# Kernel optimization log

Hardware: AMD Instinct MI355X
Metric: run time of the kernel (lower is better)

Reference implementation:

```python
import jax, jax.numpy as jnp
import numpy as np

H = 512      # hidden_size
E = 300      # embed_size
V = 50257    # output_size / vocab
B = 64       # batch
S = 128      # src_len
NEG = -1e10


def setup_inputs() -> dict:
    key = jax.random.key(0)
    ks = jax.random.split(key, 12)
    inp = {
        "input_ids": jax.random.randint(ks[0], (B,), 0, V),
        "hidden": jax.random.normal(ks[1], (B, H), jnp.float32),
        "encoder_outputs": jax.random.normal(ks[2], (S, B, 2 * H), jnp.float32),
        "mask": jax.random.randint(ks[3], (B, S), 0, 2).astype(jnp.int32),
        # parameters
        "emb_table": jax.random.normal(ks[4], (V, E), jnp.float32) * 0.02,
        "W_attn": jax.random.normal(ks[5], (H, 3 * H), jnp.float32) * 0.02,
        "b_attn": jnp.zeros((H,), jnp.float32),
        "v_w": jax.random.normal(ks[6], (1, H), jnp.float32) * 0.02,
        "W_ih": jax.random.normal(ks[7], (3 * H, 2 * H + E), jnp.float32) * 0.02,
        "W_hh": jax.random.normal(ks[8], (3 * H, H), jnp.float32) * 0.02,
        "b_ih": jnp.zeros((3 * H,), jnp.float32),
        "b_hh": jnp.zeros((3 * H,), jnp.float32),
        "W_out": jax.random.normal(ks[9], (V, 3 * H + E), jnp.float32) * 0.02,
        "b_out": jnp.zeros((V,), jnp.float32),
    }
    return inp


def reference(input_ids, hidden, encoder_outputs, mask,
              emb_table, W_attn, b_attn, v_w,
              W_ih, W_hh, b_ih, b_hh, W_out, b_out):
    # embedding lookup (dropout prob = 0 -> identity)
    embedded = emb_table[input_ids]                       # [B, E]

    # Bahdanau attention
    enc_b = jnp.transpose(encoder_outputs, (1, 0, 2))     # [B, S, 2H]
    hid_rep = jnp.broadcast_to(hidden[:, None, :], (hidden.shape[0], enc_b.shape[1], hidden.shape[1]))
    energy = jnp.tanh(jnp.concatenate([hid_rep, enc_b], axis=2) @ W_attn.T + b_attn)  # [B, S, H]
    scores = jnp.einsum('bsh,h->bs', energy, v_w[0])      # [B, S]
    scores = jnp.where(mask == 0, NEG, scores)
    a = jax.nn.softmax(scores, axis=1)                    # [B, S]

    # context vector
    weighted = jnp.einsum('bs,bse->be', a, enc_b)         # [B, 2H]

    # single-step GRU (PyTorch gate order: r, z, n)
    x = jnp.concatenate([embedded, weighted], axis=1)     # [B, E + 2H]
    gx = x @ W_ih.T + b_ih                                # [B, 3H]
    gh = hidden @ W_hh.T + b_hh                           # [B, 3H]
    h = hidden.shape[1]
    r = jax.nn.sigmoid(gx[:, :h] + gh[:, :h])
    z = jax.nn.sigmoid(gx[:, h:2*h] + gh[:, h:2*h])
    n = jnp.tanh(gx[:, 2*h:] + r * gh[:, 2*h:])
    h_new = (1.0 - z) * n + z * hidden                    # [B, H]

    # output projection
    prediction = jnp.concatenate([h_new, weighted, embedded], axis=1) @ W_out.T + b_out  # [B, V]
    return prediction, h_new, a
```

## Files before the change

### kernel.cpp

```cpp
#include <hip/hip_runtime.h>

typedef unsigned short ushort_t;
typedef short bf16x8 __attribute__((ext_vector_type(8)));
typedef float f32x4 __attribute__((ext_vector_type(4)));

#define B_ 64
#define H_ 512
#define E_ 300
#define V_ 50257
#define S_ 128

#define HNEW_OFS ((size_t)64 * 50257)
#define A_OFS    ((size_t)64 * 50257 + 64 * 512)

__device__ __forceinline__ unsigned short f2b(float f) {
  unsigned int u = __builtin_bit_cast(unsigned int, f);
  u = u + 0x7FFFu + ((u >> 16) & 1u);
  return (unsigned short)(u >> 16);
}
__device__ __forceinline__ float fast_tanh(float x) {
  x = fminf(15.f, fmaxf(-15.f, x));
  float e = __expf(-2.f * x);
  return (1.f - e) / (1.f + e);
}
__device__ __forceinline__ float fast_sigmoid(float x) {
  return 1.f / (1.f + __expf(-x));
}

template <int DT> struct Raw4;
template <> struct Raw4<0> {
  ushort4 v;
  __device__ static Raw4 zero() { return {make_ushort4(0, 0, 0, 0)}; }
};
template <> struct Raw4<1> {
  float4 v;
  __device__ static Raw4 zero() { return {make_float4(0.f, 0.f, 0.f, 0.f)}; }
};
template <int DT>
__device__ __forceinline__ Raw4<DT> ld_raw(const void* p, size_t off);
template <>
__device__ __forceinline__ Raw4<0> ld_raw<0>(const void* p, size_t off) {
  return {*(const ushort4*)((const ushort_t*)p + off)};
}
template <>
__device__ __forceinline__ Raw4<1> ld_raw<1>(const void* p, size_t off) {
  return {*(const float4*)((const float*)p + off)};
}
template <int DT>
__device__ __forceinline__ ushort4 to_b4(Raw4<DT> r);
template <>
__device__ __forceinline__ ushort4 to_b4<0>(Raw4<0> r) { return r.v; }
template <>
__device__ __forceinline__ ushort4 to_b4<1>(Raw4<1> r) {
  return make_ushort4(f2b(r.v.x), f2b(r.v.y), f2b(r.v.z), f2b(r.v.w));
}

template <int DTA, int DTW>
__global__ __launch_bounds__(256) void gemm_tile(
    const void* __restrict__ A, int lda,
    const void* __restrict__ W, int ldw, int wofs,
    const float* __restrict__ bias,
    float* __restrict__ C, int ldc,
    int M, int N, int K)
{
  __shared__ ushort_t sA[64 * 40];
  __shared__ ushort_t sB[64 * 40];
  const int tid = threadIdx.x;
  const int n0 = blockIdx.x * 64, m0 = blockIdx.y * 64;
  const int wave = tid >> 6, lane = tid & 63, quad = lane >> 4, l16 = lane & 15;

  f32x4 acc[4];
  #pragma unroll
  for (int i = 0; i < 4; ++i) acc[i] = (f32x4){0.f, 0.f, 0.f, 0.f};

  Raw4<DTA> ra[2];
  Raw4<DTW> rb[2];
  auto fetch = [&](int kt) {
    #pragma unroll
    for (int i = 0; i < 2; ++i) {
      int g = tid + i * 256;
      int row = g >> 3, gc = (g & 7) << 2;
      int gk = kt * 32 + gc;
      int ar = m0 + row, wr = n0 + row;
      ra[i] = Raw4<DTA>::zero();
      rb[i] = Raw4<DTW>::zero();
      if (gk < K && ar < M) ra[i] = ld_raw<DTA>(A, (size_t)ar * lda + gk);
      if (gk < K && wr < N) rb[i] = ld_raw<DTW>(W, (size_t)wr * ldw + wofs + gk);
    }
  };
  const int ksteps = (K + 31) >> 5;
  fetch(0);
  for (int kt = 0; kt < ksteps; ++kt) {
    #pragma unroll
    for (int i = 0; i < 2; ++i) {
      int g = tid + i * 256;
      int row = g >> 3, gc = (g & 7) << 2;
      *(ushort4*)(sA + row * 40 + gc) = to_b4<DTA>(ra[i]);
      *(ushort4*)(sB + row * 40 + gc) = to_b4<DTW>(rb[i]);
    }
    __syncthreads();
    if (kt + 1 < ksteps) fetch(kt + 1);
    bf16x8 af = *(const bf16x8*)(sA + (wave * 16 + l16) * 40 + quad * 8);
    #pragma unroll
    for (int nt = 0; nt < 4; ++nt) {
      bf16x8 bfr = *(const bf16x8*)(sB + (nt * 16 + l16) * 40 + quad * 8);
      acc[nt] = __builtin_amdgcn_mfma_f32_16x16x32_bf16(af, bfr, acc[nt], 0, 0, 0);
    }
    __syncthreads();
  }
  #pragma unroll
  for (int nt = 0; nt < 4; ++nt) {
    #pragma unroll
    for (int reg = 0; reg < 4; ++reg) {
      int row = m0 + wave * 16 + quad * 4 + reg;
      int col = n0 + nt * 16 + l16;
      if (row < M && col < N)
        C[(size_t)row * ldc + col] = acc[nt][reg] + bias[col];
    }
  }
}

__global__ __launch_bounds__(256) void attn_scores(
    const float* __restrict__ enc,
    const float* __restrict__ Wattn,
    const float* __restrict__ Gh,
    const float* __restrict__ vw,
    float* __restrict__ scores_part)
{
  __shared__ ushort_t sA[64 * 40];
  __shared__ ushort_t sB[64 * 40];
  const int tid = threadIdx.x;
  const int n0 = blockIdx.x * 64, m0 = blockIdx.y * 64;
  const int wave = tid >> 6, lane = tid & 63, quad = lane >> 4, l16 = lane & 15;

  f32x4 acc[4];
  #pragma unroll
  for (int i = 0; i < 4; ++i) acc[i] = (f32x4){0.f, 0.f, 0.f, 0.f};

  float4 ra[2], rb[2];
  auto fetch = [&](int kt) {
    #pragma unroll
    for (int i = 0; i < 2; ++i) {
      int g = tid + i * 256;
      int row = g >> 3, gc = (g & 7) << 2;
      int gk = kt * 32 + gc;
      ra[i] = *(const float4*)(enc + (size_t)(m0 + row) * 1024 + gk);
      rb[i] = *(const float4*)(Wattn + (size_t)(n0 + row) * 1536 + 512 + gk);
    }
  };
  fetch(0);
  for (int kt = 0; kt < 32; ++kt) {
    #pragma unroll
    for (int i = 0; i < 2; ++i) {
      int g = tid + i * 256;
      int row = g >> 3, gc = (g & 7) << 2;
      *(ushort4*)(sA + row * 40 + gc) =
          make_ushort4(f2b(ra[i].x), f2b(ra[i].y), f2b(ra[i].z), f2b(ra[i].w));
      *(ushort4*)(sB + row * 40 + gc) =
          make_ushort4(f2b(rb[i].x), f2b(rb[i].y), f2b(rb[i].z), f2b(rb[i].w));
    }
    __syncthreads();
    if (kt + 1 < 32) fetch(kt + 1);
    bf16x8 af = *(const bf16x8*)(sA + (wave * 16 + l16) * 40 + quad * 8);
    #pragma unroll
    for (int nt = 0; nt < 4; ++nt) {
      bf16x8 bfr = *(const bf16x8*)(sB + (nt * 16 + l16) * 40 + quad * 8);
      acc[nt] = __builtin_amdgcn_mfma_f32_16x16x32_bf16(af, bfr, acc[nt], 0, 0, 0);
    }
    __syncthreads();
  }
  float psum[4] = {0.f, 0.f, 0.f, 0.f};
  #pragma unroll
  for (int nt = 0; nt < 4; ++nt) {
    int h = n0 + nt * 16 + l16;
    float vh = vw[h];
    #pragma unroll
    for (int reg = 0; reg < 4; ++reg) {
      int r = m0 + wave * 16 + quad * 4 + reg;
      int b = r & 63;
      float e = acc[nt][reg] + Gh[b * 512 + h];
      psum[reg] += vh * fast_tanh(e);
    }
  }
  #pragma unroll
  for (int reg = 0; reg < 4; ++reg) {
    float p = psum[reg];
    p += __shfl_xor(p, 1);
    p += __shfl_xor(p, 2);
    p += __shfl_xor(p, 4);
    p += __shfl_xor(p, 8);
    if (l16 == 0) {
      int r = m0 + wave * 16 + quad * 4 + reg;
      scores_part[blockIdx.x * 8192 + r] = p;
    }
  }
}

__global__ __launch_bounds__(256) void softmax_ctx(
    const float* __restrict__ scores_part,
    const int* __restrict__ mask,
    const float* __restrict__ enc,
    const float* __restrict__ emb,
    const int* __restrict__ ids,
    float* __restrict__ out,
    ushort_t* __restrict__ x,
    ushort_t* __restrict__ xo)
{
  __shared__ float sc[128];
  __shared__ float red[128];
  const int b = blockIdx.x;
  const int tid = threadIdx.x;

  if (tid < 128) {
    float s = 0.f;
    #pragma unroll
    for (int nb = 0; nb < 8; ++nb) s += scores_part[nb * 8192 + tid * 64 + b];
    if (mask[b * 128 + tid] == 0) s = -1e10f;
    sc[tid] = s;
    red[tid] = s;
  }
  __syncthreads();
  for (int off = 64; off > 0; off >>= 1) {
    if (tid < off) red[tid] = fmaxf(red[tid], red[tid + off]);
    __syncthreads();
  }
  float m = red[0];
  __syncthreads();
  if (tid < 128) {
    float e = __expf(sc[tid] - m);
    sc[tid] = e;
    red[tid] = e;
  }
  __syncthreads();
  for (int off = 64; off > 0; off >>= 1) {
    if (tid < off) red[tid] += red[tid + off];
    __syncthreads();
  }
  float inv = 1.f / red[0];
  if (tid < 128) {
    float av = sc[tid] * inv;
    sc[tid] = av;
    out[A_OFS + b * 128 + tid] = av;
  }
  __syncthreads();

  {
    int e0 = tid * 4;
    float a0 = 0.f, a1 = 0.f, a2 = 0.f, a3 = 0.f;
    for (int s = 0; s < 128; ++s) {
      float as = sc[s];
      float4 ev = *(const float4*)(enc + (size_t)(s * 64 + b) * 1024 + e0);
      a0 += as * ev.x;
      a1 += as * ev.y;
      a2 += as * ev.z;
      a3 += as * ev.w;
    }
    ushort4 wb = make_ushort4(f2b(a0), f2b(a1), f2b(a2), f2b(a3));
    *(ushort4*)(x + b * 1344 + 300 + e0) = wb;
    *(ushort4*)(xo + b * 1856 + 512 + e0) = wb;
  }

  int rid = ids[b];
  for (int e = tid; e < 300; e += 256) {
    ushort_t h = f2b(emb[(size_t)rid * 300 + e]);
    x[b * 1344 + e] = h;
    xo[b * 1856 + 1536 + e] = h;
  }
  if (tid < 20) {
    x[b * 1344 + 1324 + tid] = 0;
    xo[b * 1856 + 1836 + tid] = 0;
  }
}

__global__ __launch_bounds__(256) void gru_pointwise(
    const float* __restrict__ gx,
    const float* __restrict__ gh,
    const float* __restrict__ hidden,
    float* __restrict__ out,
    ushort_t* __restrict__ xo)
{
  int i = blockIdx.x * 256 + threadIdx.x;
  int b = i >> 9, h = i & 511;
  float r = fast_sigmoid(gx[b * 1536 + h] + gh[b * 1536 + h]);
  float z = fast_sigmoid(gx[b * 1536 + 512 + h] + gh[b * 1536 + 512 + h]);
  float n = fast_tanh(gx[b * 1536 + 1024 + h] + r * gh[b * 1536 + 1024 + h]);
  float hp = hidden[b * 512 + h];
  float hn = (1.f - z) * n + z * hp;
  out[HNEW_OFS + b * 512 + h] = hn;
  xo[b * 1856 + h] = f2b(hn);
}

__global__ __launch_bounds__(256) void out_proj(
    const ushort_t* __restrict__ Xo,
    const float* __restrict__ Wout,
    const float* __restrict__ bout,
    float* __restrict__ pred)
{
  __shared__ ushort_t sA[64 * 40];
  __shared__ ushort_t sB[64 * 40];
  const int tid = threadIdx.x;
  const int n0 = blockIdx.x * 64;
  const int wave = tid >> 6, lane = tid & 63, quad = lane >> 4, l16 = lane & 15;

  f32x4 acc[4];
  #pragma unroll
  for (int i = 0; i < 4; ++i) acc[i] = (f32x4){0.f, 0.f, 0.f, 0.f};

  ushort4 ra[2];
  float4 rb[2];
  auto fetch = [&](int kt) {
    #pragma unroll
    for (int i = 0; i < 2; ++i) {
      int g = tid + i * 256;
      int row = g >> 3, gc = (g & 7) << 2;
      int gk = kt * 32 + gc;
      ra[i] = make_ushort4(0, 0, 0, 0);
      rb[i] = make_float4(0.f, 0.f, 0.f, 0.f);
      if (gk < 1836) {
        ra[i] = *(const ushort4*)(Xo + (size_t)row * 1856 + gk);
        int wr = n0 + row;
        if (wr < V_) rb[i] = *(const float4*)(Wout + (size_t)wr * 1836 + gk);
      }
    }
  };
  fetch(0);
  for (int kt = 0; kt < 58; ++kt) {
    #pragma unroll
    for (int i = 0; i < 2; ++i) {
      int g = tid + i * 256;
      int row = g >> 3, gc = (g & 7) << 2;
      *(ushort4*)(sA + row * 40 + gc) = ra[i];
      *(ushort4*)(sB + row * 40 + gc) =
          make_ushort4(f2b(rb[i].x), f2b(rb[i].y), f2b(rb[i].z), f2b(rb[i].w));
    }
    __syncthreads();
    if (kt + 1 < 58) fetch(kt + 1);
    bf16x8 af = *(const bf16x8*)(sA + (wave * 16 + l16) * 40 + quad * 8);
    #pragma unroll
    for (int nt = 0; nt < 4; ++nt) {
      bf16x8 bfr = *(const bf16x8*)(sB + (nt * 16 + l16) * 40 + quad * 8);
      acc[nt] = __builtin_amdgcn_mfma_f32_16x16x32_bf16(af, bfr, acc[nt], 0, 0, 0);
    }
    __syncthreads();
  }
  #pragma unroll
  for (int nt = 0; nt < 4; ++nt) {
    #pragma unroll
    for (int reg = 0; reg < 4; ++reg) {
      int row = wave * 16 + quad * 4 + reg;
      int col = n0 + nt * 16 + l16;
      if (col < V_)
        pred[(size_t)row * V_ + col] = acc[nt][reg] + bout[col];
    }
  }
}

extern "C" void kernel_launch(void* const* d_in, const int* in_sizes, int n_in,
                              void* d_out, int out_size, void* d_ws, size_t ws_size,
                              hipStream_t stream) {
  const int*   ids    = (const int*)d_in[0];
  const float* hidden = (const float*)d_in[1];
  const float* enc    = (const float*)d_in[2];
  const int*   mask   = (const int*)d_in[3];
  const float* emb    = (const float*)d_in[4];
  const float* Wattn  = (const float*)d_in[5];
  const float* battn  = (const float*)d_in[6];
  const float* vw     = (const float*)d_in[7];
  const float* Wih    = (const float*)d_in[8];
  const float* Whh    = (const float*)d_in[9];
  const float* bih    = (const float*)d_in[10];
  const float* bhh    = (const float*)d_in[11];
  const float* Wout   = (const float*)d_in[12];
  const float* bout   = (const float*)d_in[13];
  float* out = (float*)d_out;

  char* ws = (char*)d_ws;
  float*    scores_part = (float*)(ws + 0);
  float*    Gh          = (float*)(ws + 262144);
  float*    gx          = (float*)(ws + 393216);
  float*    gh          = (float*)(ws + 786432);
  ushort_t* x           = (ushort_t*)(ws + 1179648);
  ushort_t* xo          = (ushort_t*)(ws + 1351680);

  gemm_tile<1, 1><<<dim3(8, 1), 256, 0, stream>>>(
      hidden, 512, Wattn, 1536, 0, battn, Gh, 512, 64, 512, 512);

  attn_scores<<<dim3(8, 128), 256, 0, stream>>>(enc, Wattn, Gh, vw, scores_part);

  softmax_ctx<<<64, 256, 0, stream>>>(scores_part, mask, enc, emb, ids, out, x, xo);

  gemm_tile<0, 1><<<dim3(24, 1), 256, 0, stream>>>(
      x, 1344, Wih, 1324, 0, bih, gx, 1536, 64, 1536, 1324);
  gemm_tile<1, 1><<<dim3(24, 1), 256, 0, stream>>>(
      hidden, 512, Whh, 512, 0, bhh, gh, 1536, 64, 1536, 512);

  gru_pointwise<<<128, 256, 0, stream>>>(gx, gh, hidden, out, xo);

  out_proj<<<786, 256, 0, stream>>>(xo, Wout, bout, out);
}
```

Measured before the change: 720.3 us.

## Load output-projection weights straight into MFMA registers and double-buffer activations

The vocab projection kernel now loads each lane's W_out slice directly from global memory into registers in MFMA operand layout and converts it to bf16 there, so the weight tile no longer goes through LDS. Only the small activation tile is staged in LDS, now double-buffered, which allows one barrier per k-step instead of two. Each wave computes a 64x16 output slice, and the epilogue stores one column per lane. The k-tail clamps weight reads to in-bounds addresses rather than zeroing them, so correctness depends on the padded activation columns being zero.

```diff
diff --git a/kernel.cpp b/kernel.cpp
--- a/kernel.cpp
+++ b/kernel.cpp
@@ -290,67 +290,95 @@
   xo[b * 1856 + h] = f2b(hn);
 }
 
-__global__ __launch_bounds__(256) void out_proj(
+__global__ __launch_bounds__(256) void out_proj2(
     const ushort_t* __restrict__ Xo,
     const float* __restrict__ Wout,
     const float* __restrict__ bout,
     float* __restrict__ pred)
 {
-  __shared__ ushort_t sA[64 * 40];
-  __shared__ ushort_t sB[64 * 40];
+  __shared__ ushort_t sA[2][64 * 40];
   const int tid = threadIdx.x;
   const int n0 = blockIdx.x * 64;
   const int wave = tid >> 6, lane = tid & 63, quad = lane >> 4, l16 = lane & 15;
 
+  const int col = n0 + wave * 16 + l16;
+  const int colc = (col < V_) ? col : 0;
+  const float* pB = Wout + (size_t)colc * 1836;
+
+  const int arow = tid >> 2;
+  const int acol = (tid & 3) * 8;
+  const ushort_t* pA = Xo + (size_t)arow * 1856 + acol;
+  ushort_t* sAw0 = &sA[0][arow * 40 + acol];
+  ushort_t* sAw1 = &sA[1][arow * 40 + acol];
+
   f32x4 acc[4];
   #pragma unroll
   for (int i = 0; i < 4; ++i) acc[i] = (f32x4){0.f, 0.f, 0.f, 0.f};
 
-  ushort4 ra[2];
-  float4 rb[2];
-  auto fetch = [&](int kt) {
-    #pragma unroll
-    for (int i = 0; i < 2; ++i) {
-      int g = tid + i * 256;
-      int row = g >> 3, gc = (g & 7) << 2;
-      int gk = kt * 32 + gc;
-      ra[i] = make_ushort4(0, 0, 0, 0);
-      rb[i] = make_float4(0.f, 0.f, 0.f, 0.f);
-      if (gk < 1836) {
-        ra[i] = *(const ushort4*)(Xo + (size_t)row * 1856 + gk);
-        int wr = n0 + row;
-        if (wr < V_) rb[i] = *(const float4*)(Wout + (size_t)wr * 1836 + gk);
+  float4 b0a, b0b, b1a, b1b;
+  auto ldB = [&](int kt, float4& va, float4& vb) {
+    int k0 = kt * 32 + quad * 8;
+    int ka = (k0 < 1832) ? k0 : 1832;
+    int kb = (k0 + 4 < 1832) ? (k0 + 4) : 1832;
+    va = *(const float4*)(pB + ka);
+    vb = *(const float4*)(pB + kb);
+  };
+  auto packB = [](float4 a, float4 b) {
+    bf16x8 r;
+    r[0] = (short)f2b(a.x); r[1] = (short)f2b(a.y);
+    r[2] = (short)f2b(a.z); r[3] = (short)f2b(a.w);
+    r[4] = (short)f2b(b.x); r[5] = (short)f2b(b.y);
+    r[6] = (short)f2b(b.z); r[7] = (short)f2b(b.w);
+    return r;
+  };
+  auto mfma4 = [&](const ushort_t* base, bf16x8 bf) {
+    #pragma unroll
+    for (int mt = 0; mt < 4; ++mt) {
+      bf16x8 af = *(const bf16x8*)(base + (mt * 16 + l16) * 40 + quad * 8);
+      acc[mt] = __builtin_amdgcn_mfma_f32_16x16x32_bf16(af, bf, acc[mt], 0, 0, 0);
+    }
+  };
+
+  ldB(0, b0a, b0b);
+  bf16x8 aReg = *(const bf16x8*)(pA);
+  *(bf16x8*)sAw0 = aReg;
+  aReg = *(const bf16x8*)(pA + 32);
+  ldB(1, b1a, b1b);
+  __syncthreads();
+
+  #pragma unroll 1
+  for (int kt = 0; kt < 58; kt += 2) {
+    {
+      if (kt + 1 < 58) *(bf16x8*)sAw1 = aReg;
+      bf16x8 bf = packB(b0a, b0b);
+      if (kt + 2 < 58) {
+        ldB(kt + 2, b0a, b0b);
+        aReg = *(const bf16x8*)(pA + (size_t)(kt + 2) * 32);
       }
-    }
-  };
-  fetch(0);
-  for (int kt = 0; kt < 58; ++kt) {
-    #pragma unroll
-    for (int i = 0; i < 2; ++i) {
-      int g = tid + i * 256;
-      int row = g >> 3, gc = (g & 7) << 2;
-      *(ushort4*)(sA + row * 40 + gc) = ra[i];
-      *(ushort4*)(sB + row * 40 + gc) =
-          make_ushort4(f2b(rb[i].x), f2b(rb[i].y), f2b(rb[i].z), f2b(rb[i].w));
-    }
-    __syncthreads();
-    if (kt + 1 < 58) fetch(kt + 1);
-    bf16x8 af = *(const bf16x8*)(sA + (wave * 16 + l16) * 40 + quad * 8);
-    #pragma unroll
-    for (int nt = 0; nt < 4; ++nt) {
-      bf16x8 bfr = *(const bf16x8*)(sB + (nt * 16 + l16) * 40 + quad * 8);
-      acc[nt] = __builtin_amdgcn_mfma_f32_16x16x32_bf16(af, bfr, acc[nt], 0, 0, 0);
-    }
-    __syncthreads();
-  }
-  #pragma unroll
-  for (int nt = 0; nt < 4; ++nt) {
-    #pragma unroll
-    for (int reg = 0; reg < 4; ++reg) {
-      int row = wave * 16 + quad * 4 + reg;
-      int col = n0 + nt * 16 + l16;
-      if (col < V_)
-        pred[(size_t)row * V_ + col] = acc[nt][reg] + bout[col];
+      mfma4(&sA[0][0], bf);
+      __syncthreads();
+    }
+    {
+      if (kt + 3 < 58) *(bf16x8*)sAw0 = aReg;
+      bf16x8 bf = packB(b1a, b1b);
+      if (kt + 3 < 58) {
+        ldB(kt + 3, b1a, b1b);
+        aReg = *(const bf16x8*)(pA + (size_t)(kt + 3) * 32);
+      }
+      mfma4(&sA[1][0], bf);
+      __syncthreads();
+    }
+  }
+
+  if (col < V_) {
+    float bc = bout[col];
+    #pragma unroll
+    for (int mt = 0; mt < 4; ++mt) {
+      #pragma unroll
+      for (int reg = 0; reg < 4; ++reg) {
+        int prow = mt * 16 + quad * 4 + reg;
+        pred[(size_t)prow * V_ + col] = acc[mt][reg] + bc;
+      }
     }
   }
 }
@@ -396,5 +424,5 @@
 
   gru_pointwise<<<128, 256, 0, stream>>>(gx, gh, hidden, out, xo);
 
-  out_proj<<<786, 256, 0, stream>>>(xo, Wout, bout, out);
-}
+  out_proj2<<<786, 256, 0, stream>>>(xo, Wout, bout, out);
+}
```

Result: no change. 727.4 us (+1.0%).
